# Performance work log

Measured on AMD Instinct MI355X. Metric: run time of the kernel, lower is better.

Reference implementation:

```python
import jax, jax.numpy as jnp
import numpy as np
from jax import lax

N, C_IN, C_OUT, H, W = 8, 64, 64, 128, 128
K, KS, STRIDE, PAD, GROUPS = 4, 3, 1, 1, 1


def setup_inputs() -> dict:
    key = jax.random.key(0)
    ks = jax.random.split(key, 10)
    s = 0.05
    return {
        "x": jax.random.normal(ks[0], (N, C_IN, H, W), jnp.float32),
        "weight": jax.random.normal(ks[1], (K, C_OUT, C_IN // GROUPS, KS, KS), jnp.float32) * s,
        "conv_w": jax.random.normal(ks[2], (C_OUT, C_IN, KS, KS), jnp.float32) * s,
        "conv_b": jax.random.normal(ks[3], (C_OUT,), jnp.float32) * s,
        "net0_w": jax.random.normal(ks[4], (K, 1, 1, 1, 1), jnp.float32) * s,
        "net0_b": jax.random.normal(ks[5], (K,), jnp.float32) * s,
        "net1_w": jax.random.normal(ks[6], (K, 1, 3, 3, 3), jnp.float32) * s,
        "net1_b": jax.random.normal(ks[7], (K,), jnp.float32) * s,
        "net2_w": jax.random.normal(ks[8], (K, 1, 5, 3, 3), jnp.float32) * s,
        "net2_b": jax.random.normal(ks[9], (K,), jnp.float32) * s,
    }


def _conv3d_mean(x5, w, b, pad):
    # x5: (N,1,C,H,W); w: (K,1,kd,kh,kw); 'same'-style padding per kernel.
    y = lax.conv_general_dilated(x5, w, (1, 1, 1), [(p, p) for p in pad],
                                 dimension_numbers=('NCDHW', 'OIDHW', 'NCDHW'))
    # global avg pool over (C,H,W); bias is constant so add after the mean.
    return jnp.mean(y, axis=(2, 3, 4)) + b[None, :]


def reference(x, weight, conv_w, conv_b, net0_w, net0_b, net1_w, net1_b, net2_w, net2_b):
    dn2 = ('NCHW', 'OIHW', 'NCHW')
    # static residual conv branch
    r = lax.conv_general_dilated(x, conv_w, (STRIDE, STRIDE), [(PAD, PAD)] * 2,
                                 dimension_numbers=dn2) + conv_b[None, :, None, None]
    # attention over 3D convs of x.unsqueeze(1)
    x5 = x[:, None]  # (N,1,C,H,W)
    logits = (_conv3d_mean(x5, net0_w, net0_b, (0, 0, 0))
              + _conv3d_mean(x5, net1_w, net1_b, (1, 1, 1))
              + _conv3d_mean(x5, net2_w, net2_b, (2, 1, 1)))  # (N,K)
    att = jax.nn.softmax(logits, axis=-1)
    # per-sample dynamic kernel mixing: (N,K) @ (K,out,in/g,kh,kw)
    agg_w = jnp.einsum('nk,koihw->noihw', att, weight)
    # grouped conv with groups = GROUPS*N == per-sample conv (vmapped)
    def per_sample(xi, wi):
        return lax.conv_general_dilated(xi[None], wi, (STRIDE, STRIDE), [(PAD, PAD)] * 2,
                                        dimension_numbers=dn2,
                                        feature_group_count=GROUPS)[0]
    out = jax.vmap(per_sample)(x, agg_w)  # (N,out,H,W)
    return out + r
```

## Files before the change

### kernel.cpp

```cpp
#include <hip/hip_runtime.h>


typedef unsigned short ushort_t;
typedef __attribute__((ext_vector_type(8))) short bf16x8;
typedef __attribute__((ext_vector_type(4))) float f32x4;

__device__ __forceinline__ ushort_t f2bf(float f) {
    unsigned u = __float_as_uint(f);
    unsigned r = (u + 0x7fffu + ((u >> 16) & 1u)) >> 16;
    return (ushort_t)r;
}

__global__ __launch_bounds__(256) void kTR(const float* __restrict__ x,
                                           ushort_t* __restrict__ xt,
                                           float* __restrict__ cat) {
    int bid = blockIdx.x;
    int h = bid & 127, n = bid >> 7;
    int tid = threadIdx.x;
    int wg = tid & 31;
    int ci8 = tid >> 5;

    __shared__ float catloc[15];
    if (tid < 15) catloc[tid] = 0.f;
    __syncthreads();

    const float* xp = x + (size_t)(n * 64 + ci8 * 8) * 16384 + h * 128 + wg;
    float v[8][4];
#pragma unroll
    for (int j = 0; j < 8; ++j)
#pragma unroll
        for (int c = 0; c < 4; ++c)
            v[j][c] = xp[j * 16384 + c * 32];

    ushort_t* op = xt + ((size_t)((n * 128 + h) * 8 + ci8)) * 128 * 8;
#pragma unroll
    for (int c = 0; c < 4; ++c) {
        ushort_t u[8];
#pragma unroll
        for (int j = 0; j < 8; ++j) u[j] = f2bf(v[j][c]);
        uint4 pk;
        pk.x = (unsigned)u[0] | ((unsigned)u[1] << 16);
        pk.y = (unsigned)u[2] | ((unsigned)u[3] << 16);
        pk.z = (unsigned)u[4] | ((unsigned)u[5] << 16);
        pk.w = (unsigned)u[6] | ((unsigned)u[7] << 16);
        *(uint4*)(op + (size_t)(wg + c * 32) * 8) = pk;
    }

#pragma unroll
    for (int j = 0; j < 8; ++j) {
        float rs = v[j][0] + v[j][1] + v[j][2] + v[j][3];
#pragma unroll
        for (int m = 1; m <= 16; m <<= 1) rs += __shfl_xor(rs, m);
        int ci = ci8 * 8 + j;
        int cd = (ci == 0) ? 0 : (ci == 1) ? 1 : (ci == 62) ? 3 : (ci == 63) ? 4 : 2;
        if (wg == 0) {
            atomicAdd(&catloc[cd * 3 + 0], rs);
            atomicAdd(&catloc[cd * 3 + 1], v[j][0]);
        }
        if (wg == 31) atomicAdd(&catloc[cd * 3 + 2], v[j][3]);
    }
    __syncthreads();

    if (tid < 15) {
        int cd = tid / 3, st = tid % 3;
        int ch = (h == 0) ? 0 : (h == 127) ? 2 : 1;
        atomicAdd(&cat[((n * 5 + cd) * 3 + ch) * 3 + st], catloc[tid]);
    }
}

__global__ __launch_bounds__(256) void kW(const float* __restrict__ cat,
                                          const float* __restrict__ nw0, const float* __restrict__ nb0,
                                          const float* __restrict__ nw1, const float* __restrict__ nb1,
                                          const float* __restrict__ nw2, const float* __restrict__ nb2,
                                          const float* __restrict__ weight,
                                          const float* __restrict__ convw,
                                          ushort_t* __restrict__ weff) {
    int bid = blockIdx.x;
    int s = bid % 9;
    int n = bid / 9;
    int tid = threadIdx.x;

    __shared__ float box_s[45];
    __shared__ float tot_s;
    __shared__ float att_s[4];

    if (tid < 46) {
        float c[5][3][3];
#pragma unroll
        for (int i = 0; i < 5; ++i)
#pragma unroll
            for (int j = 0; j < 3; ++j)
#pragma unroll
                for (int t = 0; t < 3; ++t)
                    c[i][j][t] = cat[((n * 5 + i) * 3 + j) * 3 + t];

        if (tid < 45) {
            int dz = tid / 9 - 2;
            int dy = (tid / 3) % 3 - 1;
            int dx = tid % 3 - 1;
            float acc = 0.f;
#pragma unroll
            for (int cd = 0; cd < 5; ++cd) {
                int dv = (cd == 0) ? 0 : (cd == 1) ? 1 : (cd == 3) ? 62 : (cd == 4) ? 63 : -1;
                bool incd = (dv < 0) || (dv >= dz && dv < 64 + dz);
#pragma unroll
                for (int ch = 0; ch < 3; ++ch) {
                    int hv = (ch == 0) ? 0 : (ch == 2) ? 127 : -1;
                    bool inch = (hv < 0) || (hv >= dy && hv < 128 + dy);
                    if (incd && inch) {
                        float v = c[cd][ch][0];
                        if (dx == -1) v -= c[cd][ch][2];
                        else if (dx == 1) v -= c[cd][ch][1];
                        acc += v;
                    }
                }
            }
            box_s[tid] = acc;
        } else {
            float tot = 0.f;
#pragma unroll
            for (int i = 0; i < 5; ++i)
#pragma unroll
                for (int j = 0; j < 3; ++j) tot += c[i][j][0];
            tot_s = tot;
        }
    }
    __syncthreads();

    if (tid < 4) {
        int k = tid;
        const float invV = 1.0f / (64.f * 128.f * 128.f);
        float lg = nb0[k] + nb1[k] + nb2[k] + nw0[k] * tot_s * invV;
#pragma unroll
        for (int dz = 0; dz < 3; ++dz)
#pragma unroll
            for (int dy = 0; dy < 3; ++dy)
#pragma unroll
                for (int dx = 0; dx < 3; ++dx)
                    lg += nw1[k * 27 + dz * 9 + dy * 3 + dx] *
                          box_s[(dz + 1) * 9 + dy * 3 + dx] * invV;
#pragma unroll
        for (int b = 0; b < 45; ++b)
            lg += nw2[k * 45 + b] * box_s[b] * invV;

        float m = fmaxf(lg, __shfl_xor(lg, 1));
        m = fmaxf(m, __shfl_xor(m, 2));
        float e = __expf(lg - m);
        float ssum = e + __shfl_xor(e, 1);
        ssum += __shfl_xor(ssum, 2);
        att_s[k] = e / ssum;
    }
    __syncthreads();

    float a0 = att_s[0], a1 = att_s[1], a2 = att_s[2], a3 = att_s[3];
    int ci = tid & 63;
    int cog = tid >> 6;
    ushort_t* wp = weff + ((size_t)(n * 9 + s) * 64) * 64;
#pragma unroll
    for (int p = 0; p < 16; ++p) {
        int co = cog * 16 + p;
        size_t base = (size_t)(co * 64 + ci) * 9 + s;
        float v = convw[base]
                + a0 * weight[base]
                + a1 * weight[base +     64 * 64 * 9]
                + a2 * weight[base + 2 * 64 * 64 * 9]
                + a3 * weight[base + 3 * 64 * 64 * 9];
        wp[(size_t)co * 64 + ci] = f2bf(v);
    }
}

__global__ __launch_bounds__(256) void kC(const ushort_t* __restrict__ xt,
                                          const ushort_t* __restrict__ weff,
                                          const float* __restrict__ convb,
                                          float* __restrict__ out) {
    int bid = blockIdx.x;
    int wt = bid & 1;
    int hp = (bid >> 1) & 63;
    int n = bid >> 7;
    int h0 = hp * 2;
    int w0 = wt * 64;

    __shared__ __align__(16) ushort_t lds[4 * 8 * 66 * 8];

    int tid = threadIdx.x;
    int lane = tid & 63;
    int wave = tid >> 6;
    int kq = lane >> 4;
    int l15 = lane & 15;

    for (int idx = tid; idx < 2112; idx += 256) {
        int c = idx % 66;
        int rc8 = idx / 66;
        int r = rc8 >> 3, ci8 = rc8 & 7;
        int hg = h0 + r - 1;
        int wg = w0 + c - 1;
        uint4 vv = make_uint4(0u, 0u, 0u, 0u);
        if (hg >= 0 && hg < 128 && wg >= 0 && wg < 128)
            vv = *(const uint4*)(xt + ((size_t)((n * 128 + hg) * 8 + ci8) * 128 + wg) * 8);
        *(uint4*)&lds[(size_t)idx * 8] = vv;
    }

    int co_a = wave * 16 + l15;
    bf16x8 afrag[9][2];
#pragma unroll
    for (int s = 0; s < 9; ++s)
#pragma unroll
        for (int kc = 0; kc < 2; ++kc)
            afrag[s][kc] = *(const bf16x8*)(weff +
                ((size_t)((n * 9 + s) * 64 + co_a)) * 64 + kc * 32 + kq * 8);

    f32x4 acc[8];
#pragma unroll
    for (int nt = 0; nt < 8; ++nt) acc[nt] = (f32x4){0.f, 0.f, 0.f, 0.f};

    __syncthreads();

#pragma unroll
    for (int s = 0; s < 9; ++s) {
        int ky = s / 3, kx = s % 3;
#pragma unroll
        for (int kc = 0; kc < 2; ++kc) {
#pragma unroll
            for (int nt = 0; nt < 8; ++nt) {
                int r = nt >> 2;
                int wl = (nt & 3) * 16 + l15;
                bf16x8 bfrag = *(const bf16x8*)
                    &lds[((((r + ky) * 8 + kc * 4 + kq) * 66) + wl + kx) * 8];
                acc[nt] = __builtin_amdgcn_mfma_f32_16x16x32_bf16(
                    afrag[s][kc], bfrag, acc[nt], 0, 0, 0);
            }
        }
    }

#pragma unroll
    for (int nt = 0; nt < 8; ++nt) {
        int h = h0 + (nt >> 2);
        int w = w0 + (nt & 3) * 16 + l15;
#pragma unroll
        for (int reg = 0; reg < 4; ++reg) {
            int co = wave * 16 + kq * 4 + reg;
            float v = acc[nt][reg] + convb[co];
            out[(((size_t)n * 64 + co) * 128 + h) * 128 + w] = v;
        }
    }
}

extern "C" void kernel_launch(void* const* d_in, const int* in_sizes, int n_in,
                              void* d_out, int out_size, void* d_ws, size_t ws_size,
                              hipStream_t stream) {
    const float* x      = (const float*)d_in[0];
    const float* weight = (const float*)d_in[1];
    const float* conv_w = (const float*)d_in[2];
    const float* conv_b = (const float*)d_in[3];
    const float* n0w    = (const float*)d_in[4];
    const float* n0b    = (const float*)d_in[5];
    const float* n1w    = (const float*)d_in[6];
    const float* n1b    = (const float*)d_in[7];
    const float* n2w    = (const float*)d_in[8];
    const float* n2b    = (const float*)d_in[9];
    float* out = (float*)d_out;

    char* ws = (char*)d_ws;
    ushort_t* xt   = (ushort_t*)(ws);
    ushort_t* weff = (ushort_t*)(ws + 16777216);
    float*    cat  = (float*)(ws + 16777216 + 589824);

    hipMemsetAsync(cat, 0, 1440, stream);
    kTR<<<1024, 256, 0, stream>>>(x, xt, cat);
    kW<<<72, 256, 0, stream>>>(cat, n0w, n0b, n1w, n1b, n2w, n2b,
                               weight, conv_w, weff);
    kC<<<1024, 256, 0, stream>>>(xt, weff, conv_b, out);
}
```

Baseline: 135.3 us.

## Enlarge conv tile to four rows with LDS row reuse, drop global atomics and memset

The conv kernel now computes four output rows per block instead of two, halving the grid. It loads six input rows into LDS and reuses each B fragment across the three ky taps, so there are fewer LDS reads per MFMA and less halo overhead. The stats kernel now writes per-row partial sums instead of global atomics, and the weight kernel reduces them in shared memory, which removes the memset launch. In exchange there is a larger accumulator set and more register pressure (launch bounds set to 2 blocks), plus a bigger LDS footprint.

```diff
diff --git a/kernel.cpp b/kernel.cpp
--- a/kernel.cpp
+++ b/kernel.cpp
@@ -13,9 +13,9 @@
 
 __global__ __launch_bounds__(256) void kTR(const float* __restrict__ x,
                                            ushort_t* __restrict__ xt,
-                                           float* __restrict__ cat) {
-    int bid = blockIdx.x;
-    int h = bid & 127, n = bid >> 7;
+                                           float* __restrict__ part) {
+    int row = blockIdx.x;
+    int h = row & 127, n = row >> 7;
     int tid = threadIdx.x;
     int wg = tid & 31;
     int ci8 = tid >> 5;
@@ -32,7 +32,7 @@
         for (int c = 0; c < 4; ++c)
             v[j][c] = xp[j * 16384 + c * 32];
 
-    ushort_t* op = xt + ((size_t)((n * 128 + h) * 8 + ci8)) * 128 * 8;
+    ushort_t* op = xt + ((size_t)(row * 8 + ci8)) * 128 * 8;
 #pragma unroll
     for (int c = 0; c < 4; ++c) {
         ushort_t u[8];
@@ -60,15 +60,10 @@
         if (wg == 31) atomicAdd(&catloc[cd * 3 + 2], v[j][3]);
     }
     __syncthreads();
-
-    if (tid < 15) {
-        int cd = tid / 3, st = tid % 3;
-        int ch = (h == 0) ? 0 : (h == 127) ? 2 : 1;
-        atomicAdd(&cat[((n * 5 + cd) * 3 + ch) * 3 + st], catloc[tid]);
-    }
-}
-
-__global__ __launch_bounds__(256) void kW(const float* __restrict__ cat,
+    if (tid < 15) part[row * 16 + tid] = catloc[tid];
+}
+
+__global__ __launch_bounds__(256) void kW(const float* __restrict__ part,
                                           const float* __restrict__ nw0, const float* __restrict__ nb0,
                                           const float* __restrict__ nw1, const float* __restrict__ nb1,
                                           const float* __restrict__ nw2, const float* __restrict__ nb2,
@@ -80,10 +75,25 @@
     int n = bid / 9;
     int tid = threadIdx.x;
 
+    __shared__ float cat_s[45];
     __shared__ float box_s[45];
     __shared__ float tot_s;
     __shared__ float att_s[4];
 
+    if (tid < 45) cat_s[tid] = 0.f;
+    __syncthreads();
+    if (tid < 128) {
+        int h = tid;
+        int ch = (h == 0) ? 0 : (h == 127) ? 2 : 1;
+        const float* pp = part + (size_t)(n * 128 + h) * 16;
+#pragma unroll
+        for (int q = 0; q < 15; ++q) {
+            int cd = q / 3, st = q % 3;
+            atomicAdd(&cat_s[(cd * 3 + ch) * 3 + st], pp[q]);
+        }
+    }
+    __syncthreads();
+
     if (tid < 46) {
         float c[5][3][3];
 #pragma unroll
@@ -92,7 +102,7 @@
             for (int j = 0; j < 3; ++j)
 #pragma unroll
                 for (int t = 0; t < 3; ++t)
-                    c[i][j][t] = cat[((n * 5 + i) * 3 + j) * 3 + t];
+                    c[i][j][t] = cat_s[(i * 3 + j) * 3 + t];
 
         if (tid < 45) {
             int dz = tid / 9 - 2;
@@ -169,18 +179,18 @@
     }
 }
 
-__global__ __launch_bounds__(256) void kC(const ushort_t* __restrict__ xt,
-                                          const ushort_t* __restrict__ weff,
-                                          const float* __restrict__ convb,
-                                          float* __restrict__ out) {
+__global__ __launch_bounds__(256, 2) void kC(const ushort_t* __restrict__ xt,
+                                             const ushort_t* __restrict__ weff,
+                                             const float* __restrict__ convb,
+                                             float* __restrict__ out) {
     int bid = blockIdx.x;
     int wt = bid & 1;
-    int hp = (bid >> 1) & 63;
-    int n = bid >> 7;
-    int h0 = hp * 2;
+    int hq = (bid >> 1) & 31;
+    int n = bid >> 6;
+    int h0 = hq * 4;
     int w0 = wt * 64;
 
-    __shared__ __align__(16) ushort_t lds[4 * 8 * 66 * 8];
+    __shared__ __align__(16) ushort_t lds[6 * 8 * 66 * 8];
 
     int tid = threadIdx.x;
     int lane = tid & 63;
@@ -188,7 +198,7 @@
     int kq = lane >> 4;
     int l15 = lane & 15;
 
-    for (int idx = tid; idx < 2112; idx += 256) {
+    for (int idx = tid; idx < 3168; idx += 256) {
         int c = idx % 66;
         int rc8 = idx / 66;
         int r = rc8 >> 3, ci8 = rc8 & 7;
@@ -209,38 +219,45 @@
             afrag[s][kc] = *(const bf16x8*)(weff +
                 ((size_t)((n * 9 + s) * 64 + co_a)) * 64 + kc * 32 + kq * 8);
 
-    f32x4 acc[8];
-#pragma unroll
-    for (int nt = 0; nt < 8; ++nt) acc[nt] = (f32x4){0.f, 0.f, 0.f, 0.f};
-
-    __syncthreads();
-
-#pragma unroll
-    for (int s = 0; s < 9; ++s) {
-        int ky = s / 3, kx = s % 3;
+    f32x4 acc[16];
+#pragma unroll
+    for (int t = 0; t < 16; ++t) acc[t] = (f32x4){0.f, 0.f, 0.f, 0.f};
+
+    __syncthreads();
+
+#pragma unroll
+    for (int kx = 0; kx < 3; ++kx) {
 #pragma unroll
         for (int kc = 0; kc < 2; ++kc) {
 #pragma unroll
-            for (int nt = 0; nt < 8; ++nt) {
-                int r = nt >> 2;
-                int wl = (nt & 3) * 16 + l15;
-                bf16x8 bfrag = *(const bf16x8*)
-                    &lds[((((r + ky) * 8 + kc * 4 + kq) * 66) + wl + kx) * 8];
-                acc[nt] = __builtin_amdgcn_mfma_f32_16x16x32_bf16(
-                    afrag[s][kc], bfrag, acc[nt], 0, 0, 0);
+            for (int col = 0; col < 4; ++col) {
+                bf16x8 brow[6];
+#pragma unroll
+                for (int p = 0; p < 6; ++p)
+                    brow[p] = *(const bf16x8*)
+                        &lds[(((p * 8 + kc * 4 + kq) * 66) + col * 16 + l15 + kx) * 8];
+#pragma unroll
+                for (int ky = 0; ky < 3; ++ky)
+#pragma unroll
+                    for (int r = 0; r < 4; ++r)
+                        acc[r * 4 + col] = __builtin_amdgcn_mfma_f32_16x16x32_bf16(
+                            afrag[ky * 3 + kx][kc], brow[r + ky], acc[r * 4 + col], 0, 0, 0);
             }
         }
     }
 
 #pragma unroll
-    for (int nt = 0; nt < 8; ++nt) {
-        int h = h0 + (nt >> 2);
-        int w = w0 + (nt & 3) * 16 + l15;
-#pragma unroll
-        for (int reg = 0; reg < 4; ++reg) {
-            int co = wave * 16 + kq * 4 + reg;
-            float v = acc[nt][reg] + convb[co];
-            out[(((size_t)n * 64 + co) * 128 + h) * 128 + w] = v;
+    for (int r = 0; r < 4; ++r) {
+        int h = h0 + r;
+#pragma unroll
+        for (int col = 0; col < 4; ++col) {
+            int w = w0 + col * 16 + l15;
+#pragma unroll
+            for (int reg = 0; reg < 4; ++reg) {
+                int co = wave * 16 + kq * 4 + reg;
+                float v = acc[r * 4 + col][reg] + convb[co];
+                out[(((size_t)n * 64 + co) * 128 + h) * 128 + w] = v;
+            }
         }
     }
 }
@@ -263,11 +280,10 @@
     char* ws = (char*)d_ws;
     ushort_t* xt   = (ushort_t*)(ws);
     ushort_t* weff = (ushort_t*)(ws + 16777216);
-    float*    cat  = (float*)(ws + 16777216 + 589824);
-
-    hipMemsetAsync(cat, 0, 1440, stream);
-    kTR<<<1024, 256, 0, stream>>>(x, xt, cat);
-    kW<<<72, 256, 0, stream>>>(cat, n0w, n0b, n1w, n1b, n2w, n2b,
+    float*    part = (float*)(ws + 16777216 + 589824);
+
+    kTR<<<1024, 256, 0, stream>>>(x, xt, part);
+    kW<<<72, 256, 0, stream>>>(part, n0w, n0b, n1w, n1b, n2w, n2b,
                                weight, conv_w, weff);
-    kC<<<1024, 256, 0, stream>>>(xt, weff, conv_b, out);
-}
+    kC<<<512, 256, 0, stream>>>(xt, weff, conv_b, out);
+}
```

Result: faster. 131.9 us (-2.5%).
